# Performance work log

Hardware: AMD Instinct MI355X
Metric: run time of the kernel (lower is better)

## Reference

```python
import math
import jax, jax.numpy as jnp
import numpy as np


def _skew(X, pad_value):
    # shift every row i one step right relative to row i-1: [B,M,L] -> [B,M,M+L]
    B, M, L = X.shape
    X = jnp.pad(X, ((0, 0), (0, 0), (0, M + 1)), constant_values=pad_value)
    X = X.reshape(B, -1)[:, :-M]
    return X.reshape(B, M, M + L)


def _unskew(X):
    # reverse of _skew: [B,M,M+L] -> [B,M,L]
    B, M, ML = X.shape
    L = ML - M
    X = X.reshape(B, -1)
    X = jnp.pad(X, ((0, 0), (0, M)))
    X = X.reshape(B, M, M + L + 1)
    return X[:, :, :L]


def setup_inputs() -> dict:
    key0 = jax.random.key(0)
    k1, k2, k3, k4 = jax.random.split(key0, 4)
    BH, M, D = 64, 1024, 64          # batch*heads, block len, head dim
    L = 1024                          # attn_span
    return {
        "query": jax.random.normal(k1, (BH, M, D), dtype=jnp.float32),
        "key": jax.random.normal(k2, (BH, M + L, D), dtype=jnp.float32),
        "value": jax.random.normal(k3, (BH, M + L, D), dtype=jnp.float32),
        "key_pe": jax.random.normal(k4, (1, D, L), dtype=jnp.float32),
    }


def reference(query, key, value, key_pe):
    hidden_size = query.shape[-1]
    # content scores: [BH, M, M+L] -> banded [BH, M, L]
    attn_cont = _unskew(jnp.matmul(query, jnp.swapaxes(key, -1, -2)))
    # relative position scores: [BH, M, L] (key_pe broadcasts over batch)
    attn_pos = jnp.matmul(query, key_pe)
    attn = (attn_cont + attn_pos) / math.sqrt(hidden_size)
    attn = jax.nn.softmax(attn, axis=-1)
    # dropout p=0.0 -> identity
    attn_skew = _skew(attn, 0.0)          # [BH, M, M+L]
    out = jnp.matmul(attn_skew, value)    # [BH, M, D]
    return out
```

## Files before the change

kernel.cpp:

```cpp
#include <hip/hip_runtime.h>
#include <hip/hip_bf16.h>


typedef __attribute__((ext_vector_type(8))) short bf16x8;
typedef __attribute__((ext_vector_type(4))) short bf16x4;
typedef __attribute__((ext_vector_type(4))) float f32x4;

#define BHN   64
#define MQ    1024
#define DH    64
#define LS    1024
#define NKEY  2048
#define NTILE 17

#define SZ_PE  ((size_t)LS * DH * 2)
#define OFF_K  SZ_PE
#define SZ_K   ((size_t)BHN * NKEY * DH * 2)
#define OFF_V  (OFF_K + SZ_K)
#define SZ_V   ((size_t)BHN * DH * NKEY * 2)
#define WS_NEED (OFF_V + SZ_V)

#define SCL_LOG2E 0.18033688011112042f

__device__ __forceinline__ short f2bf(float f) {
  unsigned u = __float_as_uint(f);
  u += 0x7FFFu + ((u >> 16) & 1u);
  return (short)(u >> 16);
}
__device__ __forceinline__ float bf2f(short s) {
  return __uint_as_float(((unsigned)(unsigned short)s) << 16);
}

#if defined(__has_builtin)
#if __has_builtin(__builtin_amdgcn_cvt_pk_bf16_f32)
#define HAVE_CVT_PK 1
#endif
#endif

__device__ __forceinline__ unsigned pk2(float a, float b) {
#ifdef HAVE_CVT_PK
  auto r = __builtin_amdgcn_cvt_pk_bf16_f32(a, b);
  unsigned u;
  __builtin_memcpy(&u, &r, 4);
  return u;
#else
  return (unsigned)(unsigned short)f2bf(a) | ((unsigned)(unsigned short)f2bf(b) << 16);
#endif
}
__device__ __forceinline__ bf16x4 mk4(unsigned a, unsigned b) {
  union { unsigned u[2]; bf16x4 v; } z;
  z.u[0] = a; z.u[1] = b;
  return z.v;
}
__device__ __forceinline__ bf16x8 mk8(unsigned a, unsigned b, unsigned c, unsigned d) {
  union { unsigned u[4]; bf16x8 v; } z;
  z.u[0] = a; z.u[1] = b; z.u[2] = c; z.u[3] = d;
  return z.v;
}

__device__ __forceinline__ void wg_barrier() {
  __asm__ volatile("" ::: "memory");
  __builtin_amdgcn_s_waitcnt(0xC07F);
  __builtin_amdgcn_s_barrier();
  __asm__ volatile("" ::: "memory");
}

__global__ __launch_bounds__(256)
void prep_fused(const float* __restrict__ pe, const float* __restrict__ K,
                const float* __restrict__ V, short* __restrict__ peT,
                short* __restrict__ Kb, short* __restrict__ Vb) {
  __shared__ short st[64 * 68];
  const int bx = blockIdx.x;
  if (bx < 256) {
    const int idx = bx * 256 + threadIdx.x;
    const int rel = idx >> 6, d = idx & 63;
    peT[rel * 64 + (((d >> 3) ^ (rel & 7)) * 8) + (d & 7)] = f2bf(pe[d * LS + rel]);
  } else if (bx < 2304) {
    const size_t i = ((size_t)(bx - 256) * 256 + threadIdx.x) * 16;
    const int row = (int)(i >> 6);
    const int c16 = (int)(i & 63);
    const float4 f0 = *(const float4*)(K + i);
    const float4 f1 = *(const float4*)(K + i + 4);
    const float4 f2 = *(const float4*)(K + i + 8);
    const float4 f3 = *(const float4*)(K + i + 12);
    const bf16x8 b0 = mk8(pk2(f0.x, f0.y), pk2(f0.z, f0.w), pk2(f1.x, f1.y), pk2(f1.z, f1.w));
    const bf16x8 b1 = mk8(pk2(f2.x, f2.y), pk2(f2.z, f2.w), pk2(f3.x, f3.y), pk2(f3.z, f3.w));
    const int s7 = row & 7;
    short* dst = Kb + (size_t)row * 64;
    *(bf16x8*)&dst[(((c16 >> 3))     ^ s7) * 8] = b0;
    *(bf16x8*)&dst[(((c16 >> 3) + 1) ^ s7) * 8] = b1;
  } else {
    const int b  = bx - 2304;
    const int bh = b >> 5, jt = b & 31;
    {
      const int r = threadIdx.x >> 2, cb = (threadIdx.x & 3) * 16;
      const float* src = V + ((size_t)bh * NKEY + jt * 64 + r) * DH + cb;
#pragma unroll
      for (int c = 0; c < 16; c += 8) {
        float4 f0 = *(const float4*)(src + c);
        float4 f1 = *(const float4*)(src + c + 4);
        *(bf16x8*)&st[r * 68 + cb + c] =
            mk8(pk2(f0.x, f0.y), pk2(f0.z, f0.w), pk2(f1.x, f1.y), pk2(f1.z, f1.w));
      }
    }
    __syncthreads();
    {
      const int d = threadIdx.x >> 2, kapb = (threadIdx.x & 3) * 16;
      __attribute__((aligned(16))) short tmp[16];
#pragma unroll
      for (int j = 0; j < 16; ++j) {
        const int kap = kapb + j;
        const int k   = (kap & 3) * 16 + (kap >> 2);
        tmp[j] = st[k * 68 + d];
      }
      short* dst = Vb + ((size_t)bh * DH + d) * NKEY + jt * 64 + kapb;
      *(bf16x8*)dst       = *(bf16x8*)&tmp[0];
      *(bf16x8*)(dst + 8) = *(bf16x8*)&tmp[8];
    }
  }
}

template <bool PRECONV>
__global__ __launch_bounds__(256, 4)
void seq_attn_kernel(const float* __restrict__ Qf, const float* __restrict__ Kf,
                     const float* __restrict__ Vf, const short* __restrict__ peT,
                     const short* __restrict__ Kb, const short* __restrict__ Vb,
                     float* __restrict__ Out) {
  __shared__ short sK[64 * 64];
  __shared__ short sPE[2 * 64 * 64];
  __shared__ short sV[64 * 64];
  __shared__ short sPA[64 * 64];

  const int tid  = threadIdx.x;
  const int w    = tid >> 6;
  const int lane = tid & 63;
  const int li   = lane & 15;
  const int quad = lane >> 4;
  const int linear = blockIdx.y * 16 + blockIdx.x;
  const int slot   = linear >> 3;
  const int bh     = (linear & 7) * 8 + (slot >> 4);
  const int i0     = (slot & 15) * 64;
  const int rbase  = w * 16 + quad * 4;

  bf16x8 aq[2];
  {
    const float* qp = Qf + (size_t)((bh * MQ + i0 + w * 16 + li) * DH) + quad * 8;
#pragma unroll
    for (int ks = 0; ks < 2; ++ks) {
      float4 f0 = *(const float4*)(qp + ks * 32);
      float4 f1 = *(const float4*)(qp + ks * 32 + 4);
      f0.x *= SCL_LOG2E; f0.y *= SCL_LOG2E; f0.z *= SCL_LOG2E; f0.w *= SCL_LOG2E;
      f1.x *= SCL_LOG2E; f1.y *= SCL_LOG2E; f1.z *= SCL_LOG2E; f1.w *= SCL_LOG2E;
      aq[ks] = mk8(pk2(f0.x, f0.y), pk2(f0.z, f0.w), pk2(f1.x, f1.y), pk2(f1.z, f1.w));
    }
  }

  float l_i[4] = {0.f, 0.f, 0.f, 0.f};
  f32x4 acco[4];
#pragma unroll
  for (int nt = 0; nt < 4; ++nt) acco[nt] = (f32x4){0.f, 0.f, 0.f, 0.f};

  f32x4 curPw[4];
  f32x4 prevw3 = (f32x4){0.f, 0.f, 0.f, 0.f};

  const int slot0 = w * 128 + lane;
  short* wrK  = sK  + slot0 * 8;
  short* wrV  = sV  + slot0 * 8;
  short* wrP0 = sPE + slot0 * 8;
  short* wrP1 = sPE + 4096 + slot0 * 8;
  const int vs0d = slot0 >> 3, vs0g = (slot0 & 7) ^ (vs0d & 7);
  const int s1 = slot0 + 64;
  const int vs1d = s1 >> 3,  vs1g = (s1 & 7) ^ (vs1d & 7);
  const short* gK  = Kb + ((size_t)bh * NKEY + i0) * 64 + slot0 * 8;
  const short* gV0 = Vb + ((size_t)bh * DH + vs0d) * NKEY + i0 + vs0g * 8;
  const short* gV1 = Vb + ((size_t)bh * DH + vs1d) * NKEY + i0 + vs1g * 8;
  const short* gPE = peT + slot0 * 8;

  bf16x8 kpf0, kpf1, vpf0, vpf1, ppf0, ppf1;
  if constexpr (PRECONV) {
    kpf0 = *(const bf16x8*)gK;  kpf1 = *(const bf16x8*)(gK + 512);  gK += 4096;
    vpf0 = *(const bf16x8*)gV0; vpf1 = *(const bf16x8*)gV1;  gV0 += 64; gV1 += 64;
    ppf0 = *(const bf16x8*)gPE; ppf1 = *(const bf16x8*)(gPE + 512); gPE += 4096;
  }

  for (int t = 0; t < NTILE; ++t) {
    const int j0 = i0 + t * 64;
    wg_barrier();

    if constexpr (PRECONV) {
      *(bf16x8*)wrK         = kpf0;
      *(bf16x8*)(wrK + 512) = kpf1;
      *(bf16x8*)wrV         = vpf0;
      *(bf16x8*)(wrV + 512) = vpf1;
      if (t < NTILE - 1) {
        short* wp = (t & 1) ? wrP1 : wrP0;
        *(bf16x8*)wp         = ppf0;
        *(bf16x8*)(wp + 512) = ppf1;
      }
      if (t + 1 < NTILE) {
        kpf0 = *(const bf16x8*)gK;  kpf1 = *(const bf16x8*)(gK + 512);  gK += 4096;
        vpf0 = *(const bf16x8*)gV0; vpf1 = *(const bf16x8*)gV1;  gV0 += 64; gV1 += 64;
      }
      if (t + 1 < NTILE - 1) {
        ppf0 = *(const bf16x8*)gPE; ppf1 = *(const bf16x8*)(gPE + 512); gPE += 4096;
      }
    } else {
      {
        const int srow = tid >> 2, l0 = tid & 3, sdb = l0 * 16;
        const float* src = Kf + (size_t)(bh * NKEY + j0 + srow) * DH + sdb;
        const float4 a0 = *(const float4*)(src + 0);
        const float4 a1 = *(const float4*)(src + 4);
        const float4 a2 = *(const float4*)(src + 8);
        const float4 a3 = *(const float4*)(src + 12);
        const bf16x8 b0 = mk8(pk2(a0.x, a0.y), pk2(a0.z, a0.w), pk2(a1.x, a1.y), pk2(a1.z, a1.w));
        const bf16x8 b1 = mk8(pk2(a2.x, a2.y), pk2(a2.z, a2.w), pk2(a3.x, a3.y), pk2(a3.z, a3.w));
        const int s7 = srow & 7;
        *(bf16x8*)&sK[srow * 64 + (((2 * l0)     ^ s7) * 8)] = b0;
        *(bf16x8*)&sK[srow * 64 + (((2 * l0 + 1) ^ s7) * 8)] = b1;
      }
      {
        const int vdb = (tid & 15) * 4, vkb = (tid >> 4) * 4;
        const float* src = Vf + (size_t)(bh * NKEY + j0 + vkb) * DH + vdb;
#pragma unroll
        for (int m = 0; m < 4; ++m) {
          const float4 rr = *(const float4*)(src + m * DH);
          const int k   = vkb + m;
          const int kap = (k & 15) * 4 + (k >> 4);
#pragma unroll
          for (int jj = 0; jj < 4; ++jj) {
            const int d = vdb + jj;
            const float fv = (jj == 0) ? rr.x : (jj == 1) ? rr.y : (jj == 2) ? rr.z : rr.w;
            sV[d * 64 + (((kap >> 3) ^ (d & 7)) * 8) + (kap & 7)] = f2bf(fv);
          }
        }
      }
      if (t < NTILE - 1) {
        const short* src = peT + (size_t)t * 64 * 64;
        short* db = sPE + (size_t)(t & 1) * 4096;
        *(bf16x8*)&db[tid * 16]     = *(const bf16x8*)(src + tid * 16);
        *(bf16x8*)&db[tid * 16 + 8] = *(const bf16x8*)(src + tid * 16 + 8);
      }
    }
    wg_barrier();

#pragma unroll
    for (int m = 0; m < 4; ++m) {
      const int colIdx = 4 * t - w + m;
      const int base = ((colIdx >> 2) & 1) * 4096 + ((colIdx & 3) * 16 + li) * 64;
      f32x4 c = (f32x4){0.f, 0.f, 0.f, 0.f};
#pragma unroll
      for (int ks = 0; ks < 2; ++ks) {
        const int gs = (((ks * 4 + quad) ^ (li & 7)) * 8);
        const bf16x8 b = *(bf16x8*)&sPE[base + gs];
        c = __builtin_amdgcn_mfma_f32_16x16x32_bf16(aq[ks], b, c, 0, 0, 0);
      }
      curPw[m] = c;
    }

    f32x4 cs[4];
#pragma unroll
    for (int nt = 0; nt < 4; ++nt) {
      f32x4 c = (f32x4){0.f, 0.f, 0.f, 0.f};
#pragma unroll
      for (int ks = 0; ks < 2; ++ks) {
        const int gs = (((ks * 4 + quad) ^ (li & 7)) * 8);
        const bf16x8 b = *(bf16x8*)&sK[(nt * 16 + li) * 64 + gs];
        c = __builtin_amdgcn_mfma_f32_16x16x32_bf16(aq[ks], b, c, 0, 0, 0);
      }
      cs[nt] = c;
    }

#pragma unroll
    for (int r = 0; r < 4; ++r) {
      const int e       = li - quad * 4 - r;
      const bool ge     = (e >= 0);
      const int srcLane = quad * 16 + (e & 15);
      const float shm = __shfl(prevw3[r], srcLane);
      const unsigned pk01 = pk2(curPw[0][r], curPw[1][r]);
      const unsigned pk23 = pk2(curPw[2][r], curPw[3][r]);
      const unsigned s01 = (unsigned)__shfl((int)pk01, srcLane);
      const unsigned s23 = (unsigned)__shfl((int)pk23, srcLane);
      const float sh0 = bf2f((short)(s01 & 0xffffu));
      const float sh1 = bf2f((short)(s01 >> 16));
      const float sh2 = bf2f((short)(s23 & 0xffffu));
      const float sh3 = bf2f((short)(s23 >> 16));
      const float pos0 = ge ? sh0 : shm;
      const float pos1 = ge ? sh1 : sh0;
      const float pos2 = ge ? sh2 : sh1;
      const float pos3 = ge ? sh3 : sh2;
      float p0 = __builtin_exp2f(cs[0][r] + pos0);
      float p1 = __builtin_exp2f(cs[1][r] + pos1);
      float p2 = __builtin_exp2f(cs[2][r] + pos2);
      float p3 = __builtin_exp2f(cs[3][r] + pos3);
      if (t == 0) {
        p0 = (0 > w || (0 == w && ge)) ? p0 : 0.f;
        p1 = (1 > w || (1 == w && ge)) ? p1 : 0.f;
        p2 = (2 > w || (2 == w && ge)) ? p2 : 0.f;
        p3 = (3 > w || (3 == w && ge)) ? p3 : 0.f;
      } else if (t == NTILE - 1) {
        p0 = (0 < w || (0 == w && !ge)) ? p0 : 0.f;
        p1 = (1 < w || (1 == w && !ge)) ? p1 : 0.f;
        p2 = (2 < w || (2 == w && !ge)) ? p2 : 0.f;
        p3 = (3 < w || (3 == w && !ge)) ? p3 : 0.f;
      }
      l_i[r] += (p0 + p1) + (p2 + p3);
      const int rowA = rbase + r;
      const bf16x4 pkv = mk4(pk2(p0, p1), pk2(p2, p3));
      *(bf16x4*)&sPA[rowA * 64 + (((li >> 1) ^ (rowA & 7)) * 8) + (li & 1) * 4] = pkv;
    }
    prevw3 = curPw[3];

#pragma unroll
    for (int ks = 0; ks < 2; ++ks) {
      const int rowA = w * 16 + li;
      const bf16x8 ap =
          *(bf16x8*)&sPA[rowA * 64 + (((ks * 4 + quad) ^ (rowA & 7)) * 8)];
#pragma unroll
      for (int nt = 0; nt < 4; ++nt) {
        const int d  = nt * 16 + li;
        const int gs = (((ks * 4 + quad) ^ (d & 7)) * 8);
        const bf16x8 bv = *(bf16x8*)&sV[d * 64 + gs];
        acco[nt] = __builtin_amdgcn_mfma_f32_16x16x32_bf16(ap, bv, acco[nt], 0, 0, 0);
      }
    }
  }

#pragma unroll
  for (int r = 0; r < 4; ++r) {
    float l = l_i[r];
    l += __shfl_xor(l, 1);
    l += __shfl_xor(l, 2);
    l += __shfl_xor(l, 4);
    l += __shfl_xor(l, 8);
    const float inv = 1.0f / l;
#pragma unroll
    for (int nt = 0; nt < 4; ++nt) {
      Out[(size_t)(bh * MQ + i0 + rbase + r) * DH + nt * 16 + li] = acco[nt][r] * inv;
    }
  }
}

extern "C" void kernel_launch(void* const* d_in, const int* in_sizes, int n_in,
                              void* d_out, int out_size, void* d_ws, size_t ws_size,
                              hipStream_t stream) {
  const float* q  = (const float*)d_in[0];
  const float* k  = (const float*)d_in[1];
  const float* v  = (const float*)d_in[2];
  const float* pe = (const float*)d_in[3];
  float* out = (float*)d_out;
  short* peT = (short*)d_ws;
  short* Kb  = (short*)((char*)d_ws + OFF_K);
  short* Vb  = (short*)((char*)d_ws + OFF_V);
  const bool preconv = ws_size >= WS_NEED;

  dim3 grid(MQ / 64, BHN);
  if (preconv) {
    prep_fused<<<4352, 256, 0, stream>>>(pe, k, v, peT, Kb, Vb);
    seq_attn_kernel<true><<<grid, 256, 0, stream>>>(q, k, v, peT, Kb, Vb, out);
  } else {
    prep_fused<<<256, 256, 0, stream>>>(pe, k, v, peT, Kb, Vb);
    seq_attn_kernel<false><<<grid, 256, 0, stream>>>(q, k, v, peT, Kb, Vb, out);
  }
}
```

Measured before the change: 181.9 us.

## Load K, V and PE tiles straight into LDS with async global_load_lds

Replaces the register-staged software prefetch of K, V and PE tiles with direct global-to-LDS async copies issued after the first barrier of each tile, and swaps the custom barrier for __syncthreads. It also switches exp2 to the raw hardware builtin. This frees prefetch registers and removes the LDS store instructions. In exchange the next tile is no longer prefetched during compute, so load latency is exposed between the two barriers.

```diff
diff --git a/kernel.cpp b/kernel.cpp
--- a/kernel.cpp
+++ b/kernel.cpp
@@ -35,7 +35,18 @@
 #if __has_builtin(__builtin_amdgcn_cvt_pk_bf16_f32)
 #define HAVE_CVT_PK 1
 #endif
-#endif
+#if __has_builtin(__builtin_amdgcn_exp2f)
+#define HAVE_EXP2 1
+#endif
+#endif
+
+__device__ __forceinline__ float fast_exp2(float x) {
+#ifdef HAVE_EXP2
+  return __builtin_amdgcn_exp2f(x);
+#else
+  return __builtin_exp2f(x);
+#endif
+}
 
 __device__ __forceinline__ unsigned pk2(float a, float b) {
 #ifdef HAVE_CVT_PK
@@ -57,12 +68,9 @@
   z.u[0] = a; z.u[1] = b; z.u[2] = c; z.u[3] = d;
   return z.v;
 }
-
-__device__ __forceinline__ void wg_barrier() {
-  __asm__ volatile("" ::: "memory");
-  __builtin_amdgcn_s_waitcnt(0xC07F);
-  __builtin_amdgcn_s_barrier();
-  __asm__ volatile("" ::: "memory");
+__device__ __forceinline__ void async_copy16(const void* g, void* l) {
+  __builtin_amdgcn_global_load_lds((const __attribute__((address_space(1))) void*)g,
+                                   (__attribute__((address_space(3))) void*)l, 16, 0, 0);
 }
 
 __global__ __launch_bounds__(256)
@@ -163,46 +171,37 @@
   f32x4 curPw[4];
   f32x4 prevw3 = (f32x4){0.f, 0.f, 0.f, 0.f};
 
-  const int slot0 = w * 128 + lane;
-  short* wrK  = sK  + slot0 * 8;
-  short* wrV  = sV  + slot0 * 8;
-  short* wrP0 = sPE + slot0 * 8;
-  short* wrP1 = sPE + 4096 + slot0 * 8;
-  const int vs0d = slot0 >> 3, vs0g = (slot0 & 7) ^ (vs0d & 7);
-  const int s1 = slot0 + 64;
-  const int vs1d = s1 >> 3,  vs1g = (s1 & 7) ^ (vs1d & 7);
-  const short* gK  = Kb + ((size_t)bh * NKEY + i0) * 64 + slot0 * 8;
-  const short* gV0 = Vb + ((size_t)bh * DH + vs0d) * NKEY + i0 + vs0g * 8;
-  const short* gV1 = Vb + ((size_t)bh * DH + vs1d) * NKEY + i0 + vs1g * 8;
-  const short* gPE = peT + slot0 * 8;
-
-  bf16x8 kpf0, kpf1, vpf0, vpf1, ppf0, ppf1;
-  if constexpr (PRECONV) {
-    kpf0 = *(const bf16x8*)gK;  kpf1 = *(const bf16x8*)(gK + 512);  gK += 4096;
-    vpf0 = *(const bf16x8*)gV0; vpf1 = *(const bf16x8*)gV1;  gV0 += 64; gV1 += 64;
-    ppf0 = *(const bf16x8*)gPE; ppf1 = *(const bf16x8*)(gPE + 512); gPE += 4096;
-  }
-
   for (int t = 0; t < NTILE; ++t) {
     const int j0 = i0 + t * 64;
-    wg_barrier();
+    __syncthreads();
 
     if constexpr (PRECONV) {
-      *(bf16x8*)wrK         = kpf0;
-      *(bf16x8*)(wrK + 512) = kpf1;
-      *(bf16x8*)wrV         = vpf0;
-      *(bf16x8*)(wrV + 512) = vpf1;
+      {
+        const char* gb = (const char*)(Kb + ((size_t)bh * NKEY + j0) * 64);
+#pragma unroll
+        for (int it = 0; it < 2; ++it) {
+          const int c0 = w * 128 + it * 64;
+          async_copy16(gb + (size_t)(c0 + lane) * 16, (char*)sK + (size_t)c0 * 16);
+        }
+      }
       if (t < NTILE - 1) {
-        short* wp = (t & 1) ? wrP1 : wrP0;
-        *(bf16x8*)wp         = ppf0;
-        *(bf16x8*)(wp + 512) = ppf1;
-      }
-      if (t + 1 < NTILE) {
-        kpf0 = *(const bf16x8*)gK;  kpf1 = *(const bf16x8*)(gK + 512);  gK += 4096;
-        vpf0 = *(const bf16x8*)gV0; vpf1 = *(const bf16x8*)gV1;  gV0 += 64; gV1 += 64;
-      }
-      if (t + 1 < NTILE - 1) {
-        ppf0 = *(const bf16x8*)gPE; ppf1 = *(const bf16x8*)(gPE + 512); gPE += 4096;
+        const char* gb = (const char*)(peT + (size_t)t * 64 * 64);
+        char* db = (char*)sPE + (size_t)(t & 1) * 8192;
+#pragma unroll
+        for (int it = 0; it < 2; ++it) {
+          const int c0 = w * 128 + it * 64;
+          async_copy16(gb + (size_t)(c0 + lane) * 16, db + (size_t)c0 * 16);
+        }
+      }
+      {
+#pragma unroll
+        for (int it = 0; it < 2; ++it) {
+          const int s = w * 128 + it * 64 + lane;
+          const int d = s >> 3;
+          const int g = (s & 7) ^ (d & 7);
+          const short* gp = Vb + ((size_t)bh * DH + d) * NKEY + j0 + g * 8;
+          async_copy16(gp, (char*)sV + (size_t)(w * 128 + it * 64) * 16);
+        }
       }
     } else {
       {
@@ -241,7 +240,7 @@
         *(bf16x8*)&db[tid * 16 + 8] = *(const bf16x8*)(src + tid * 16 + 8);
       }
     }
-    wg_barrier();
+    __syncthreads();
 
 #pragma unroll
     for (int m = 0; m < 4; ++m) {
@@ -288,10 +287,10 @@
       const float pos1 = ge ? sh1 : sh0;
       const float pos2 = ge ? sh2 : sh1;
       const float pos3 = ge ? sh3 : sh2;
-      float p0 = __builtin_exp2f(cs[0][r] + pos0);
-      float p1 = __builtin_exp2f(cs[1][r] + pos1);
-      float p2 = __builtin_exp2f(cs[2][r] + pos2);
-      float p3 = __builtin_exp2f(cs[3][r] + pos3);
+      float p0 = fast_exp2(cs[0][r] + pos0);
+      float p1 = fast_exp2(cs[1][r] + pos1);
+      float p2 = fast_exp2(cs[2][r] + pos2);
+      float p3 = fast_exp2(cs[3][r] + pos3);
       if (t == 0) {
         p0 = (0 > w || (0 == w && ge)) ? p0 : 0.f;
         p1 = (1 > w || (1 == w && ge)) ? p1 : 0.f;
```

Result: faster. 173.4 us (-4.7%).
